# Optimization experiments

Measured on AMD Instinct MI355X. Metric: run time of the kernel, lower is better.

The kernel has to match this reference:

```python
import jax, jax.numpy as jnp
import numpy as np

EMBED = 512
HEADS = 8
HEAD_DIM = EMBED // HEADS


def setup_inputs() -> dict:
    key = jax.random.key(0)
    ks = jax.random.split(key, 7)
    N, S = 2, 4096
    inp = {
        "input_v": jax.random.normal(ks[0], (N, S, EMBED), jnp.float32),
        "input_q": jax.random.normal(ks[1], (N, S, EMBED), jnp.float32),
        "input_k": jax.random.normal(ks[2], (N, S, EMBED), jnp.float32),
        # nn.Linear weights stored as [out, in]; y = x @ W.T
        "W_Q": jax.random.normal(ks[3], (EMBED, EMBED), jnp.float32) / np.sqrt(EMBED),
        "W_K": jax.random.normal(ks[4], (EMBED, EMBED), jnp.float32) / np.sqrt(EMBED),
        "W_V": jax.random.normal(ks[5], (EMBED, EMBED), jnp.float32) / np.sqrt(EMBED),
        "W_fc": jax.random.normal(ks[6], (EMBED, EMBED), jnp.float32) / np.sqrt(EMBED),
    }
    return inp


def reference(input_v, input_q, input_k, W_Q, W_K, W_V, W_fc):
    N, Sq, _ = input_q.shape
    Sk = input_k.shape[1]
    Sv = input_v.shape[1]
    # projections (no bias), reshape to heads
    q = (input_q @ W_Q.T).reshape(N, Sq, HEADS, HEAD_DIM)
    k = (input_k @ W_K.T).reshape(N, Sk, HEADS, HEAD_DIM)
    v = (input_v @ W_V.T).reshape(N, Sv, HEADS, HEAD_DIM)
    # NOTE: original scales by sqrt(embed_size), not sqrt(head_dim)
    scale = 1.0 / jnp.sqrt(jnp.asarray(EMBED, q.dtype))
    energy = jnp.einsum("nqhd,nkhd->nhqk", q, k) * scale  # [N,H,Q,K]
    attn = jax.nn.softmax(energy, axis=-1)
    out = jnp.einsum("nhqk,nkhd->nqhd", attn, v).reshape(N, Sq, EMBED)
    return out @ W_fc.T
```

## Files before the change

kernel.cpp:

```cpp
#include <hip/hip_runtime.h>
#include <hip/hip_bf16.h>
#include <stdint.h>

typedef unsigned short u16;
typedef unsigned int u32;
typedef __attribute__((ext_vector_type(8))) short bf16x8;
typedef __attribute__((ext_vector_type(4))) float f32x4;
typedef __attribute__((ext_vector_type(16))) float f32x16;
typedef __attribute__((ext_vector_type(4))) u32 u32x4;

#define SEQ    4096
#define EMB    512
#define HEADS  8
#define HDIM   64
#define NBATCH 2

__device__ __forceinline__ u16 f2bf(float f) {
  unsigned u = __builtin_bit_cast(unsigned, f);
  u += 0x7fffu + ((u >> 16) & 1u);
  return (u16)(u >> 16);
}

__device__ __forceinline__ void gld_lds16(const void* g, void* lds) {
  __builtin_amdgcn_global_load_lds(
      (const __attribute__((address_space(1))) unsigned int*)(uintptr_t)g,
      (__attribute__((address_space(3))) unsigned int*)(uint32_t)(uintptr_t)lds,
      16, 0, 0);
}

#define CVT_PK(lo, hi) ({ u32 _r; \
  asm("v_cvt_pk_bf16_f32 %0, %1, %2" : "=v"(_r) : "v"(lo), "v"(hi)); _r; })

template <bool XBF16>
__device__ __forceinline__ void gemm512_tile(const void* __restrict__ Xv,
                                             const float* __restrict__ W,
                                             u16* lA, u16* lB,
                                             int m0, int n0,
                                             f32x4 acc[4][4]) {
  const int tid  = threadIdx.x;
  const int lane = tid & 63;
  const int wid  = tid >> 6;
  const int wr   = wid >> 1, wc = wid & 1;

  for (int k0 = 0; k0 < EMB; k0 += 32) {
    __syncthreads();
    if constexpr (XBF16) {
      const u16* X = (const u16*)Xv;
      const int srow = lane >> 2;
      const int soff = (lane & 3) * 8;
#pragma unroll
      for (int i = 0; i < 2; ++i) {
        int rbase = wid * 32 + i * 16;
        gld_lds16(X + (size_t)(m0 + rbase + srow) * EMB + k0 + soff, lA + rbase * 32);
      }
    } else {
      const float* X = (const float*)Xv;
#pragma unroll
      for (int i = 0; i < 4; ++i) {
        int chunk = i * 256 + tid;
        int row = chunk >> 3;
        int c4  = (chunk & 7) * 4;
        float4 v = *(const float4*)(X + (size_t)(m0 + row) * EMB + k0 + c4);
        ushort4 b;
        b.x = f2bf(v.x); b.y = f2bf(v.y); b.z = f2bf(v.z); b.w = f2bf(v.w);
        *(ushort4*)(lA + row * 32 + c4) = b;
      }
    }
#pragma unroll
    for (int i = 0; i < 4; ++i) {
      int chunk = i * 256 + tid;
      int row = chunk >> 3;
      int c4  = (chunk & 7) * 4;
      float4 v = *(const float4*)(W + (size_t)(n0 + row) * EMB + k0 + c4);
      ushort4 b;
      b.x = f2bf(v.x); b.y = f2bf(v.y); b.z = f2bf(v.z); b.w = f2bf(v.w);
      *(ushort4*)(lB + row * 32 + c4) = b;
    }
    __syncthreads();

    bf16x8 a[4], b[4];
#pragma unroll
    for (int t = 0; t < 4; ++t) {
      a[t] = *(const bf16x8*)(lA + (wr * 64 + t * 16 + (lane & 15)) * 32 + (lane >> 4) * 8);
      b[t] = *(const bf16x8*)(lB + (wc * 64 + t * 16 + (lane & 15)) * 32 + (lane >> 4) * 8);
    }
#pragma unroll
    for (int mr = 0; mr < 4; ++mr)
#pragma unroll
      for (int nc = 0; nc < 4; ++nc)
        acc[mr][nc] = __builtin_amdgcn_mfma_f32_16x16x32_bf16(a[mr], b[nc], acc[mr][nc], 0, 0, 0);
  }
}

__global__ __launch_bounds__(256, 2) void k_proj_qkv(
    const float* __restrict__ xq, const float* __restrict__ xk, const float* __restrict__ xv,
    const float* __restrict__ wq, const float* __restrict__ wk, const float* __restrict__ wv,
    u16* __restrict__ yq, u16* __restrict__ yk, u16* __restrict__ yv) {
  __shared__ u16 lA[128 * 32];
  __shared__ u16 lB[128 * 32];
  const int z = blockIdx.z;
  const int lane = threadIdx.x & 63, wid = threadIdx.x >> 6;
  const int wr = wid >> 1, wc = wid & 1;

  if (z == 2) {
    const int m0 = blockIdx.y * 128, n0 = blockIdx.x * 128;
    f32x4 acc[4][4] = {};
    gemm512_tile<false>(wv, xv, lA, lB, m0, n0, acc);
#pragma unroll
    for (int mr = 0; mr < 4; ++mr)
#pragma unroll
      for (int nc = 0; nc < 4; ++nc)
#pragma unroll
        for (int j = 0; j < 4; ++j) {
          int m = m0 + wr * 64 + mr * 16 + (lane >> 4) * 4 + j;
          int c = n0 + wc * 64 + nc * 16 + (lane & 15);
          int hh = m >> 6, d = m & 63;
          int n = c >> 12, s = c & (SEQ - 1);
          yv[(((size_t)(n * HEADS + hh)) * HDIM + d) * SEQ + s] = f2bf(acc[mr][nc][j]);
        }
    return;
  }

  const float* X = (z == 0) ? xq : xk;
  const float* W = (z == 0) ? wq : wk;
  u16* Y         = (z == 0) ? yq : yk;
  const float oscale = (z == 0) ? 0.06375873f : 1.0f;
  const int m0 = blockIdx.x * 128, n0 = blockIdx.y * 128;

  f32x4 acc[4][4] = {};
  gemm512_tile<false>(X, W, lA, lB, m0, n0, acc);

#pragma unroll
  for (int mr = 0; mr < 4; ++mr)
#pragma unroll
    for (int nc = 0; nc < 4; ++nc)
#pragma unroll
      for (int j = 0; j < 4; ++j) {
        int m = m0 + wr * 64 + mr * 16 + (lane >> 4) * 4 + j;
        int c = n0 + wc * 64 + nc * 16 + (lane & 15);
        int n = m >> 12, s = m & (SEQ - 1);
        int hh = c >> 6, d = c & 63;
        Y[(((size_t)(n * HEADS + hh)) * SEQ + s) * HDIM + d] = f2bf(acc[mr][nc][j] * oscale);
      }
}

__global__ __launch_bounds__(256, 2) void k_proj_out(
    const u16* __restrict__ X, const float* __restrict__ W, float* __restrict__ Y) {
  __shared__ u16 lA[128 * 32];
  __shared__ u16 lB[128 * 32];
  const int m0 = blockIdx.x * 128, n0 = blockIdx.y * 128;
  f32x4 acc[4][4] = {};
  gemm512_tile<true>(X, W, lA, lB, m0, n0, acc);

  const int lane = threadIdx.x & 63, wid = threadIdx.x >> 6;
  const int wr = wid >> 1, wc = wid & 1;
#pragma unroll
  for (int mr = 0; mr < 4; ++mr)
#pragma unroll
    for (int nc = 0; nc < 4; ++nc)
#pragma unroll
      for (int j = 0; j < 4; ++j) {
        int m = m0 + wr * 64 + mr * 16 + (lane >> 4) * 4 + j;
        int c = n0 + wc * 64 + nc * 16 + (lane & 15);
        Y[(size_t)m * EMB + c] = acc[mr][nc][j];
      }
}

template <bool PART>
__global__ __launch_bounds__(256, 2) void k_attn(
    const u16* __restrict__ Qg, const u16* __restrict__ Kg,
    const u16* __restrict__ Vt, u16* __restrict__ Og,
    float* __restrict__ pO, float* __restrict__ pML) {
  __shared__ u16 lK[2][64 * 64];
  __shared__ u16 lV[2][64 * 64];

  int flat = blockIdx.x + 32 * blockIdx.y + (PART ? 512 * blockIdx.z : 0);
  int xcd = flat & 7, i = flat >> 3;
  int bx, nh, bz;
  if constexpr (PART) {
    nh = xcd + 8 * (i >> 6);
    int rem = i & 63;
    bz = rem >> 5;
    bx = rem & 31;
  } else {
    nh = xcd + 8 * (i >> 5);
    bx = i & 31;
    bz = 0;
  }

  const int tid = threadIdx.x, lane = tid & 63, wid = tid >> 6;
  const int l31 = lane & 31, h = lane >> 5;
  const int q0 = bx * 128 + wid * 32;
  const int kvb = PART ? bz * (SEQ / 2) : 0;
  const int NT  = PART ? (SEQ / 128) : (SEQ / 64);

  const u16* Qh = Qg + (size_t)nh * SEQ * HDIM;
  const u16* Kh = Kg + (size_t)nh * SEQ * HDIM;
  const u16* Vh = Vt + (size_t)nh * HDIM * SEQ;

  bf16x8 qf[4];
#pragma unroll
  for (int t = 0; t < 4; ++t)
    qf[t] = *(const bf16x8*)&Qh[(size_t)(q0 + l31) * HDIM + t * 16 + h * 8];

  const u32x4 ones4 = {0x3F803F80u, 0x3F803F80u, 0x3F803F80u, 0x3F803F80u};
  const bf16x8 onesf = __builtin_bit_cast(bf16x8, ones4);

  f32x16 o0 = {}, o1 = {};
  f32x16 lacc = {};

  auto stage = [&](int buf, int kv0) {
#pragma unroll
    for (int i2 = 0; i2 < 2; ++i2) {
      int g = i2 * 256 + tid;
      int kr = g >> 3, kc = g & 7;
      int krp = (kr & 0x33) | ((kr & 4) << 1) | ((kr & 8) >> 1);
      gld_lds16(Kh + (size_t)(kv0 + krp) * HDIM + ((kc ^ (kr & 7)) * 8),
                &lK[buf][g * 8]);
    }
#pragma unroll
    for (int i2 = 0; i2 < 2; ++i2) {
      int g = i2 * 256 + tid;
      int vd = g >> 3, vc = g & 7;
      gld_lds16(Vh + (size_t)vd * SEQ + kv0 + ((vc ^ (vd & 7)) * 8),
                &lV[buf][g * 8]);
    }
  };

  stage(0, kvb);
  asm volatile("s_waitcnt vmcnt(0)" ::: "memory");
  __syncthreads();

  for (int t = 0; t < NT; ++t) {
    const int cur = t & 1, nxt = cur ^ 1;
    if (t < NT - 1) stage(nxt, kvb + (t + 1) * 64);

    f32x16 sA = {}, sB = {};
    __builtin_amdgcn_s_setprio(1);
#pragma unroll
    for (int tt = 0; tt < 4; ++tt) {
      int co = (tt * 16 + h * 8) ^ ((l31 & 7) << 3);
      bf16x8 k0 = *(const bf16x8*)&lK[cur][l31 * 64 + co];
      bf16x8 k1 = *(const bf16x8*)&lK[cur][(32 + l31) * 64 + co];
      sA = __builtin_amdgcn_mfma_f32_32x32x16_bf16(k0, qf[tt], sA, 0, 0, 0);
      sB = __builtin_amdgcn_mfma_f32_32x32x16_bf16(k1, qf[tt], sB, 0, 0, 0);
    }
    __builtin_amdgcn_s_setprio(0);

#pragma unroll
    for (int r = 0; r < 16; ++r) {
      sA[r] = exp2f(sA[r]);
      sB[r] = exp2f(sB[r]);
    }

    u32x4 pfr[4];
#pragma unroll
    for (int w = 0; w < 4; ++w) {
      pfr[0][w] = CVT_PK(sA[2 * w],     sA[2 * w + 1]);
      pfr[1][w] = CVT_PK(sA[8 + 2 * w], sA[8 + 2 * w + 1]);
      pfr[2][w] = CVT_PK(sB[2 * w],     sB[2 * w + 1]);
      pfr[3][w] = CVT_PK(sB[8 + 2 * w], sB[8 + 2 * w + 1]);
    }

#pragma unroll
    for (int tt = 0; tt < 4; ++tt)
      lacc = __builtin_amdgcn_mfma_f32_32x32x16_bf16(
          onesf, __builtin_bit_cast(bf16x8, pfr[tt]), lacc, 0, 0, 0);

#pragma unroll
    for (int dt = 0; dt < 2; ++dt) {
      bf16x8 vf[4];
#pragma unroll
      for (int tt = 0; tt < 4; ++tt) {
        int d = dt * 32 + l31;
        vf[tt] = *(const bf16x8*)&lV[cur][d * 64 + (((tt * 2 + h) ^ (d & 7)) * 8)];
      }
      __builtin_amdgcn_s_setprio(1);
#pragma unroll
      for (int tt = 0; tt < 4; ++tt) {
        bf16x8 pb = __builtin_bit_cast(bf16x8, pfr[tt]);
        if (dt == 0) o0 = __builtin_amdgcn_mfma_f32_32x32x16_bf16(vf[tt], pb, o0, 0, 0, 0);
        else         o1 = __builtin_amdgcn_mfma_f32_32x32x16_bf16(vf[tt], pb, o1, 0, 0, 0);
      }
      __builtin_amdgcn_s_setprio(0);
    }

    asm volatile("s_waitcnt vmcnt(0)" ::: "memory");
    __syncthreads();
  }

  const int q = q0 + l31;
  if constexpr (!PART) {
    const float linv = 1.f / lacc[0];
    const int n = nh >> 3, hh = nh & 7;
#pragma unroll
    for (int r = 0; r < 16; ++r) {
      int row = (r & 3) + 8 * (r >> 2) + 4 * h;
      Og[((size_t)(n * SEQ + q)) * EMB + hh * 64 + row] = f2bf(o0[r] * linv);
      Og[((size_t)(n * SEQ + q)) * EMB + hh * 64 + 32 + row] = f2bf(o1[r] * linv);
    }
  } else {
    const size_t PO_STRIDE = (size_t)16 * SEQ * HDIM;
    float* po = pO + bz * PO_STRIDE + ((size_t)nh * SEQ + q) * HDIM;
#pragma unroll
    for (int g = 0; g < 4; ++g) {
      float4 a = {o0[4 * g + 0], o0[4 * g + 1], o0[4 * g + 2], o0[4 * g + 3]};
      float4 b = {o1[4 * g + 0], o1[4 * g + 1], o1[4 * g + 2], o1[4 * g + 3]};
      *(float4*)(po + 8 * g + 4 * h) = a;
      *(float4*)(po + 32 + 8 * g + 4 * h) = b;
    }
    if (h == 0) {
      float2 ml = {0.0f, lacc[0]};
      *(float2*)(pML + ((size_t)bz * 16 * SEQ + (size_t)nh * SEQ + q) * 2) = ml;
    }
  }
}

__global__ __launch_bounds__(256) void k_merge(const float* __restrict__ pO,
                                               const float* __restrict__ pML,
                                               u16* __restrict__ aws) {
  const int idx = blockIdx.x * 256 + threadIdx.x;
  const int row = idx >> 4;
  const int ch  = idx & 15;
  const float2 ml1 = ((const float2*)pML)[row];
  const float2 ml2 = ((const float2*)pML)[16 * SEQ + row];
  float M = fmaxf(ml1.x, ml2.x);
  float w1 = __expf(ml1.x - M), w2 = __expf(ml2.x - M);
  float inv = 1.f / fmaf(w1, ml1.y, w2 * ml2.y);
  w1 *= inv; w2 *= inv;
  const size_t PO_STRIDE4 = (size_t)16 * SEQ * HDIM / 4;
  const float4 a = ((const float4*)pO)[idx];
  const float4 b = ((const float4*)pO)[PO_STRIDE4 + idx];
  ushort4 r;
  r.x = f2bf(w1 * a.x + w2 * b.x);
  r.y = f2bf(w1 * a.y + w2 * b.y);
  r.z = f2bf(w1 * a.z + w2 * b.z);
  r.w = f2bf(w1 * a.w + w2 * b.w);
  const int nh = row >> 12, q = row & (SEQ - 1);
  const int n = nh >> 3, hh = nh & 7;
  *(ushort4*)&aws[((size_t)(n * SEQ + q)) * EMB + hh * 64 + ch * 4] = r;
}

extern "C" void kernel_launch(void* const* d_in, const int* in_sizes, int n_in,
                              void* d_out, int out_size, void* d_ws, size_t ws_size,
                              hipStream_t stream) {
  const float* xv  = (const float*)d_in[0];
  const float* xq  = (const float*)d_in[1];
  const float* xk  = (const float*)d_in[2];
  const float* wq  = (const float*)d_in[3];
  const float* wk  = (const float*)d_in[4];
  const float* wv  = (const float*)d_in[5];
  const float* wfc = (const float*)d_in[6];
  float* out = (float*)d_out;
  u16* ws    = (u16*)d_ws;

  const size_t PSZ = (size_t)NBATCH * HEADS * SEQ * HDIM;
  if (ws_size < 4 * PSZ * sizeof(u16)) return;
  u16* qws = ws;
  u16* kws = ws + PSZ;
  u16* vws = ws + 2 * PSZ;
  u16* aws = ws + 3 * PSZ;

  const size_t base    = 4 * PSZ * sizeof(u16);
  const size_t poBytes = 2ull * 16 * SEQ * HDIM * sizeof(float);
  const size_t mlBytes = 2ull * 16 * SEQ * 2 * sizeof(float);
  const bool   split   = ws_size >= base + poBytes + mlBytes;
  float* pO  = (float*)((char*)d_ws + base);
  float* pML = (float*)((char*)d_ws + base + poBytes);

  k_proj_qkv<<<dim3(64, 4, 3), 256, 0, stream>>>(xq, xk, xv, wq, wk, wv, qws, kws, vws);
  if (split) {
    k_attn<true><<<dim3(32, 16, 2), 256, 0, stream>>>(qws, kws, vws, aws, pO, pML);
    k_merge<<<4096, 256, 0, stream>>>(pO, pML, aws);
  } else {
    k_attn<false><<<dim3(32, 16, 1), 256, 0, stream>>>(qws, kws, vws, aws, nullptr, nullptr);
  }
  k_proj_out<<<dim3(64, 4), 256, 0, stream>>>(aws, wfc, out);
}
```

Measured before the change: 157.0 us.

## Split KV four ways with bf16 partials, pre-convert QKV weights to bf16

Attention KV splitting now uses a templated split count, four by default. Partial outputs are stored as bf16 instead of fp32, and the max/sum pair becomes a single sum, since no running max is used. A new kernel converts W_Q/W_K/W_V to bf16 once so the projection GEMM can load weights directly into LDS, and exp2f is replaced by a raw v_exp_f32. The wall buffer aliases pOb, which is safe only because projection finishes before attention writes partials. The aim is more parallelism and less traffic, at the cost of an extra launch and extra bf16 rounding of partials.

Measured after the change: 141.5 us. 1.11x faster.

```diff
diff --git a/kernel.cpp b/kernel.cpp
--- a/kernel.cpp
+++ b/kernel.cpp
@@ -20,6 +20,9 @@
   u += 0x7fffu + ((u >> 16) & 1u);
   return (u16)(u >> 16);
 }
+__device__ __forceinline__ float bf2f(u16 x) {
+  return __builtin_bit_cast(float, (u32)x << 16);
+}
 
 __device__ __forceinline__ void gld_lds16(const void* g, void* lds) {
   __builtin_amdgcn_global_load_lds(
@@ -31,9 +34,11 @@
 #define CVT_PK(lo, hi) ({ u32 _r; \
   asm("v_cvt_pk_bf16_f32 %0, %1, %2" : "=v"(_r) : "v"(lo), "v"(hi)); _r; })
 
-template <bool XBF16>
-__device__ __forceinline__ void gemm512_tile(const void* __restrict__ Xv,
-                                             const float* __restrict__ W,
+#define EXP2(x) ({ float _r; asm("v_exp_f32 %0, %1" : "=v"(_r) : "v"(x)); _r; })
+
+template <bool ABF16, bool BBF16>
+__device__ __forceinline__ void gemm512_tile(const void* __restrict__ Av,
+                                             const void* __restrict__ Bv,
                                              u16* lA, u16* lB,
                                              int m0, int n0,
                                              f32x4 acc[4][4]) {
@@ -41,20 +46,20 @@
   const int lane = tid & 63;
   const int wid  = tid >> 6;
   const int wr   = wid >> 1, wc = wid & 1;
+  const int srow = lane >> 2;
+  const int soff = (lane & 3) * 8;
 
   for (int k0 = 0; k0 < EMB; k0 += 32) {
     __syncthreads();
-    if constexpr (XBF16) {
-      const u16* X = (const u16*)Xv;
-      const int srow = lane >> 2;
-      const int soff = (lane & 3) * 8;
+    if constexpr (ABF16) {
+      const u16* X = (const u16*)Av;
 #pragma unroll
       for (int i = 0; i < 2; ++i) {
         int rbase = wid * 32 + i * 16;
         gld_lds16(X + (size_t)(m0 + rbase + srow) * EMB + k0 + soff, lA + rbase * 32);
       }
     } else {
-      const float* X = (const float*)Xv;
+      const float* X = (const float*)Av;
 #pragma unroll
       for (int i = 0; i < 4; ++i) {
         int chunk = i * 256 + tid;
@@ -66,15 +71,25 @@
         *(ushort4*)(lA + row * 32 + c4) = b;
       }
     }
-#pragma unroll
-    for (int i = 0; i < 4; ++i) {
-      int chunk = i * 256 + tid;
-      int row = chunk >> 3;
-      int c4  = (chunk & 7) * 4;
-      float4 v = *(const float4*)(W + (size_t)(n0 + row) * EMB + k0 + c4);
-      ushort4 b;
-      b.x = f2bf(v.x); b.y = f2bf(v.y); b.z = f2bf(v.z); b.w = f2bf(v.w);
-      *(ushort4*)(lB + row * 32 + c4) = b;
+    if constexpr (BBF16) {
+      const u16* W = (const u16*)Bv;
+#pragma unroll
+      for (int i = 0; i < 2; ++i) {
+        int rbase = wid * 32 + i * 16;
+        gld_lds16(W + (size_t)(n0 + rbase + srow) * EMB + k0 + soff, lB + rbase * 32);
+      }
+    } else {
+      const float* W = (const float*)Bv;
+#pragma unroll
+      for (int i = 0; i < 4; ++i) {
+        int chunk = i * 256 + tid;
+        int row = chunk >> 3;
+        int c4  = (chunk & 7) * 4;
+        float4 v = *(const float4*)(W + (size_t)(n0 + row) * EMB + k0 + c4);
+        ushort4 b;
+        b.x = f2bf(v.x); b.y = f2bf(v.y); b.z = f2bf(v.z); b.w = f2bf(v.w);
+        *(ushort4*)(lB + row * 32 + c4) = b;
+      }
     }
     __syncthreads();
 
@@ -92,9 +107,25 @@
   }
 }
 
+__global__ __launch_bounds__(256) void k_wconv(
+    const float* __restrict__ wq, const float* __restrict__ wk,
+    const float* __restrict__ wv, u16* __restrict__ wall) {
+  const int t = blockIdx.x * 256 + threadIdx.x;
+  const int w = t >> 15, off = (t & 32767) * 8;
+  const float* src = (w == 0) ? wq : (w == 1) ? wk : wv;
+  u16* dst = wall + (size_t)w * EMB * EMB + off;
+#pragma unroll
+  for (int i = 0; i < 2; ++i) {
+    float4 v = *(const float4*)(src + (size_t)w * 0 + off + i * 4);
+    ushort4 b;
+    b.x = f2bf(v.x); b.y = f2bf(v.y); b.z = f2bf(v.z); b.w = f2bf(v.w);
+    *(ushort4*)(dst + i * 4) = b;
+  }
+}
+
 __global__ __launch_bounds__(256, 2) void k_proj_qkv(
     const float* __restrict__ xq, const float* __restrict__ xk, const float* __restrict__ xv,
-    const float* __restrict__ wq, const float* __restrict__ wk, const float* __restrict__ wv,
+    const u16* __restrict__ wall,
     u16* __restrict__ yq, u16* __restrict__ yk, u16* __restrict__ yv) {
   __shared__ u16 lA[128 * 32];
   __shared__ u16 lB[128 * 32];
@@ -105,7 +136,7 @@
   if (z == 2) {
     const int m0 = blockIdx.y * 128, n0 = blockIdx.x * 128;
     f32x4 acc[4][4] = {};
-    gemm512_tile<false>(wv, xv, lA, lB, m0, n0, acc);
+    gemm512_tile<true, false>(wall + 2 * EMB * EMB, xv, lA, lB, m0, n0, acc);
 #pragma unroll
     for (int mr = 0; mr < 4; ++mr)
 #pragma unroll
@@ -122,13 +153,13 @@
   }
 
   const float* X = (z == 0) ? xq : xk;
-  const float* W = (z == 0) ? wq : wk;
+  const u16* W   = wall + (size_t)z * EMB * EMB;
   u16* Y         = (z == 0) ? yq : yk;
   const float oscale = (z == 0) ? 0.06375873f : 1.0f;
   const int m0 = blockIdx.x * 128, n0 = blockIdx.y * 128;
 
   f32x4 acc[4][4] = {};
-  gemm512_tile<false>(X, W, lA, lB, m0, n0, acc);
+  gemm512_tile<false, true>(X, W, lA, lB, m0, n0, acc);
 
 #pragma unroll
   for (int mr = 0; mr < 4; ++mr)
@@ -150,7 +181,7 @@
   __shared__ u16 lB[128 * 32];
   const int m0 = blockIdx.x * 128, n0 = blockIdx.y * 128;
   f32x4 acc[4][4] = {};
-  gemm512_tile<true>(X, W, lA, lB, m0, n0, acc);
+  gemm512_tile<true, false>(X, W, lA, lB, m0, n0, acc);
 
   const int lane = threadIdx.x & 63, wid = threadIdx.x >> 6;
   const int wr = wid >> 1, wc = wid & 1;
@@ -166,33 +197,26 @@
       }
 }
 
-template <bool PART>
+template <int S>
 __global__ __launch_bounds__(256, 2) void k_attn(
     const u16* __restrict__ Qg, const u16* __restrict__ Kg,
     const u16* __restrict__ Vt, u16* __restrict__ Og,
-    float* __restrict__ pO, float* __restrict__ pML) {
+    u16* __restrict__ pOb, float* __restrict__ pL) {
   __shared__ u16 lK[2][64 * 64];
   __shared__ u16 lV[2][64 * 64];
-
-  int flat = blockIdx.x + 32 * blockIdx.y + (PART ? 512 * blockIdx.z : 0);
+  constexpr int LS = (S == 4) ? 2 : (S == 2) ? 1 : 0;
+
+  int flat = blockIdx.x + 32 * blockIdx.y + 512 * blockIdx.z;
   int xcd = flat & 7, i = flat >> 3;
-  int bx, nh, bz;
-  if constexpr (PART) {
-    nh = xcd + 8 * (i >> 6);
-    int rem = i & 63;
-    bz = rem >> 5;
-    bx = rem & 31;
-  } else {
-    nh = xcd + 8 * (i >> 5);
-    bx = i & 31;
-    bz = 0;
-  }
+  int bx = i & 31;
+  int bz = (S > 1) ? ((i >> 5) & (S - 1)) : 0;
+  int nh = xcd + 8 * (i >> (5 + LS));
 
   const int tid = threadIdx.x, lane = tid & 63, wid = tid >> 6;
   const int l31 = lane & 31, h = lane >> 5;
   const int q0 = bx * 128 + wid * 32;
-  const int kvb = PART ? bz * (SEQ / 2) : 0;
-  const int NT  = PART ? (SEQ / 128) : (SEQ / 64);
+  const int kvb = bz * (SEQ / S);
+  const int NT  = SEQ / S / 64;
 
   const u16* Qh = Qg + (size_t)nh * SEQ * HDIM;
   const u16* Kh = Kg + (size_t)nh * SEQ * HDIM;
@@ -249,8 +273,8 @@
 
 #pragma unroll
     for (int r = 0; r < 16; ++r) {
-      sA[r] = exp2f(sA[r]);
-      sB[r] = exp2f(sB[r]);
+      sA[r] = EXP2(sA[r]);
+      sB[r] = EXP2(sB[r]);
     }
 
     u32x4 pfr[4];
@@ -290,7 +314,7 @@
   }
 
   const int q = q0 + l31;
-  if constexpr (!PART) {
+  if constexpr (S == 1) {
     const float linv = 1.f / lacc[0];
     const int n = nh >> 3, hh = nh & 7;
 #pragma unroll
@@ -300,45 +324,50 @@
       Og[((size_t)(n * SEQ + q)) * EMB + hh * 64 + 32 + row] = f2bf(o1[r] * linv);
     }
   } else {
-    const size_t PO_STRIDE = (size_t)16 * SEQ * HDIM;
-    float* po = pO + bz * PO_STRIDE + ((size_t)nh * SEQ + q) * HDIM;
+    const size_t PO_E = (size_t)16 * SEQ * HDIM;
+    u16* po = pOb + (size_t)bz * PO_E + ((size_t)nh * SEQ + q) * HDIM;
 #pragma unroll
     for (int g = 0; g < 4; ++g) {
-      float4 a = {o0[4 * g + 0], o0[4 * g + 1], o0[4 * g + 2], o0[4 * g + 3]};
-      float4 b = {o1[4 * g + 0], o1[4 * g + 1], o1[4 * g + 2], o1[4 * g + 3]};
-      *(float4*)(po + 8 * g + 4 * h) = a;
-      *(float4*)(po + 32 + 8 * g + 4 * h) = b;
-    }
-    if (h == 0) {
-      float2 ml = {0.0f, lacc[0]};
-      *(float2*)(pML + ((size_t)bz * 16 * SEQ + (size_t)nh * SEQ + q) * 2) = ml;
-    }
-  }
-}
-
-__global__ __launch_bounds__(256) void k_merge(const float* __restrict__ pO,
-                                               const float* __restrict__ pML,
+      ushort4 a = {f2bf(o0[4 * g + 0]), f2bf(o0[4 * g + 1]),
+                   f2bf(o0[4 * g + 2]), f2bf(o0[4 * g + 3])};
+      ushort4 b = {f2bf(o1[4 * g + 0]), f2bf(o1[4 * g + 1]),
+                   f2bf(o1[4 * g + 2]), f2bf(o1[4 * g + 3])};
+      *(ushort4*)(po + 8 * g + 4 * h) = a;
+      *(ushort4*)(po + 32 + 8 * g + 4 * h) = b;
+    }
+    if (h == 0)
+      pL[(size_t)bz * 16 * SEQ + (size_t)nh * SEQ + q] = lacc[0];
+  }
+}
+
+template <int S>
+__global__ __launch_bounds__(256) void k_merge(const u16* __restrict__ pOb,
+                                               const float* __restrict__ pL,
                                                u16* __restrict__ aws) {
   const int idx = blockIdx.x * 256 + threadIdx.x;
-  const int row = idx >> 4;
-  const int ch  = idx & 15;
-  const float2 ml1 = ((const float2*)pML)[row];
-  const float2 ml2 = ((const float2*)pML)[16 * SEQ + row];
-  float M = fmaxf(ml1.x, ml2.x);
-  float w1 = __expf(ml1.x - M), w2 = __expf(ml2.x - M);
-  float inv = 1.f / fmaf(w1, ml1.y, w2 * ml2.y);
-  w1 *= inv; w2 *= inv;
-  const size_t PO_STRIDE4 = (size_t)16 * SEQ * HDIM / 4;
-  const float4 a = ((const float4*)pO)[idx];
-  const float4 b = ((const float4*)pO)[PO_STRIDE4 + idx];
-  ushort4 r;
-  r.x = f2bf(w1 * a.x + w2 * b.x);
-  r.y = f2bf(w1 * a.y + w2 * b.y);
-  r.z = f2bf(w1 * a.z + w2 * b.z);
-  r.w = f2bf(w1 * a.w + w2 * b.w);
+  const int row = idx >> 3;
+  const int ch  = idx & 7;
+  float l = 0.f;
+#pragma unroll
+  for (int s = 0; s < S; ++s) l += pL[(size_t)s * 16 * SEQ + row];
+  const float inv = 1.f / l;
+  float acc[8] = {};
+  const size_t PO_E = (size_t)16 * SEQ * HDIM;
+#pragma unroll
+  for (int s = 0; s < S; ++s) {
+    const u16* p = pOb + (size_t)s * PO_E + (size_t)row * HDIM + ch * 8;
+    ushort4 a = *(const ushort4*)p;
+    ushort4 b = *(const ushort4*)(p + 4);
+    acc[0] += bf2f(a.x); acc[1] += bf2f(a.y); acc[2] += bf2f(a.z); acc[3] += bf2f(a.w);
+    acc[4] += bf2f(b.x); acc[5] += bf2f(b.y); acc[6] += bf2f(b.z); acc[7] += bf2f(b.w);
+  }
+  ushort4 r0 = {f2bf(acc[0] * inv), f2bf(acc[1] * inv), f2bf(acc[2] * inv), f2bf(acc[3] * inv)};
+  ushort4 r1 = {f2bf(acc[4] * inv), f2bf(acc[5] * inv), f2bf(acc[6] * inv), f2bf(acc[7] * inv)};
   const int nh = row >> 12, q = row & (SEQ - 1);
   const int n = nh >> 3, hh = nh & 7;
-  *(ushort4*)&aws[((size_t)(n * SEQ + q)) * EMB + hh * 64 + ch * 4] = r;
+  u16* dst = aws + ((size_t)(n * SEQ + q)) * EMB + hh * 64 + ch * 8;
+  *(ushort4*)dst = r0;
+  *(ushort4*)(dst + 4) = r1;
 }
 
 extern "C" void kernel_launch(void* const* d_in, const int* in_sizes, int n_in,
@@ -354,26 +383,35 @@
   float* out = (float*)d_out;
   u16* ws    = (u16*)d_ws;
 
-  const size_t PSZ = (size_t)NBATCH * HEADS * SEQ * HDIM;
-  if (ws_size < 4 * PSZ * sizeof(u16)) return;
+  const size_t PSZ  = (size_t)NBATCH * HEADS * SEQ * HDIM;
+  const size_t PO_E = (size_t)16 * SEQ * HDIM;
+  if (ws_size < 4 * PSZ * sizeof(u16) + 3 * EMB * EMB * sizeof(u16)) return;
+
   u16* qws = ws;
   u16* kws = ws + PSZ;
   u16* vws = ws + 2 * PSZ;
   u16* aws = ws + 3 * PSZ;
-
-  const size_t base    = 4 * PSZ * sizeof(u16);
-  const size_t poBytes = 2ull * 16 * SEQ * HDIM * sizeof(float);
-  const size_t mlBytes = 2ull * 16 * SEQ * 2 * sizeof(float);
-  const bool   split   = ws_size >= base + poBytes + mlBytes;
-  float* pO  = (float*)((char*)d_ws + base);
-  float* pML = (float*)((char*)d_ws + base + poBytes);
-
-  k_proj_qkv<<<dim3(64, 4, 3), 256, 0, stream>>>(xq, xk, xv, wq, wk, wv, qws, kws, vws);
-  if (split) {
-    k_attn<true><<<dim3(32, 16, 2), 256, 0, stream>>>(qws, kws, vws, aws, pO, pML);
-    k_merge<<<4096, 256, 0, stream>>>(pO, pML, aws);
+  u16* wall = ws + 4 * PSZ;
+  u16* pOb  = ws + 4 * PSZ;
+
+  const size_t base = 4 * PSZ * sizeof(u16);
+  const size_t need4 = base + 4 * PO_E * 2 + 4 * (size_t)16 * SEQ * 4;
+  const size_t need2 = base + 2 * PO_E * 2 + 2 * (size_t)16 * SEQ * 4;
+
+  k_wconv<<<384, 256, 0, stream>>>(wq, wk, wv, wall);
+  k_proj_qkv<<<dim3(64, 4, 3), 256, 0, stream>>>(xq, xk, xv, wall, qws, kws, vws);
+
+  if (ws_size >= need4) {
+    float* pL = (float*)((char*)d_ws + base + 4 * PO_E * 2);
+    k_attn<4><<<dim3(32, 16, 4), 256, 0, stream>>>(qws, kws, vws, aws, pOb, pL);
+    k_merge<4><<<2048, 256, 0, stream>>>(pOb, pL, aws);
+  } else if (ws_size >= need2) {
+    float* pL = (float*)((char*)d_ws + base + 2 * PO_E * 2);
+    k_attn<2><<<dim3(32, 16, 2), 256, 0, stream>>>(qws, kws, vws, aws, pOb, pL);
+    k_merge<2><<<2048, 256, 0, stream>>>(pOb, pL, aws);
   } else {
-    k_attn<false><<<dim3(32, 16, 1), 256, 0, stream>>>(qws, kws, vws, aws, nullptr, nullptr);
-  }
+    k_attn<1><<<dim3(32, 16, 1), 256, 0, stream>>>(qws, kws, vws, aws, nullptr, nullptr);
+  }
+
   k_proj_out<<<dim3(64, 4), 256, 0, stream>>>(aws, wfc, out);
 }
```
